# Optimization experiments

Hardware: AMD Instinct MI355X
Metric: run time of the kernel (lower is better)

## Reference

```python
import jax, jax.numpy as jnp
import numpy as np

# ---- larq ste_sign: forward = sign (0 -> +1), backward = clipped straight-through ----
def _sign(x):
    return jnp.where(x >= 0, jnp.ones_like(x), -jnp.ones_like(x))

@jax.custom_vjp
def ste_sign(x):
    return _sign(x)

def _ste_fwd(x):
    return _sign(x), x

def _ste_bwd(x, g):
    return (g * (jnp.abs(x) <= 1.0).astype(g.dtype),)

ste_sign.defvjp(_ste_fwd, _ste_bwd)

BN_EPS = 1e-3  # keras BatchNormalization default epsilon

def conv2d(x, w, padding):
    # x: NHWC, w: HWIO
    return jax.lax.conv_general_dilated(
        x, w, window_strides=(1, 1), padding=padding,
        dimension_numbers=('NHWC', 'HWIO', 'NHWC'))

def maxpool2(x):
    return jax.lax.reduce_window(x, -jnp.inf, jax.lax.max,
                                 (1, 2, 2, 1), (1, 2, 2, 1), 'VALID')

def batchnorm(x, mean, var, beta):
    # BatchNormalization(scale=False): gamma fixed at 1
    return (x - mean) * jax.lax.rsqrt(var + BN_EPS) + beta


def setup_inputs() -> dict:
    key = jax.random.key(0)
    ks = jax.random.split(key, 20)
    d = {}
    d['x'] = jax.random.normal(ks[0], (64, 128, 128, 3), dtype=jnp.float32)
    d['w1'] = jax.random.normal(ks[1], (3, 3, 3, 32), dtype=jnp.float32)
    d['m1'] = jax.random.normal(ks[2], (32,), dtype=jnp.float32)
    d['v1'] = jax.random.uniform(ks[3], (32,), dtype=jnp.float32)
    d['b1'] = jax.random.normal(ks[4], (32,), dtype=jnp.float32)
    d['w2'] = jax.random.normal(ks[5], (3, 3, 32, 64), dtype=jnp.float32)
    d['m2'] = jax.random.normal(ks[6], (64,), dtype=jnp.float32)
    d['v2'] = jax.random.uniform(ks[7], (64,), dtype=jnp.float32)
    d['b2'] = jax.random.normal(ks[8], (64,), dtype=jnp.float32)
    d['w3'] = jax.random.normal(ks[9], (3, 3, 64, 128), dtype=jnp.float32)
    d['m3'] = jax.random.normal(ks[10], (128,), dtype=jnp.float32)
    d['v3'] = jax.random.uniform(ks[11], (128,), dtype=jnp.float32)
    d['b3'] = jax.random.normal(ks[12], (128,), dtype=jnp.float32)
    d['w4'] = jax.random.normal(ks[13], (3, 3, 128, 256), dtype=jnp.float32)
    d['m4'] = jax.random.normal(ks[14], (256,), dtype=jnp.float32)
    d['v4'] = jax.random.uniform(ks[15], (256,), dtype=jnp.float32)
    d['b4'] = jax.random.normal(ks[16], (256,), dtype=jnp.float32)
    return d


def reference(x, w1, m1, v1, b1, w2, m2, v2, b2, w3, m3, v3, b3, w4, m4, v4, b4):
    # Stem: QuantConv2D(32,3x3,valid) with kernel quantized only (no input quantizer)
    y = conv2d(x, ste_sign(w1), 'VALID')          # [B,126,126,32]
    y = batchnorm(maxpool2(y), m1, v1, b1)        # [B,63,63,32]
    # Three binarized blocks: ste_sign(input) conv ste_sign(kernel), same padding
    for w, m, v, b in ((w2, m2, v2, b2), (w3, m3, v3, b3), (w4, m4, v4, b4)):
        y = conv2d(ste_sign(y), ste_sign(w), 'SAME')
        y = batchnorm(maxpool2(y), m, v, b)       # halves spatial dims
    return y                                      # [B,7,7,256]
```

## Files before the change

### kernel.cpp

```cpp
#include <hip/hip_runtime.h>
#include <stdint.h>

#define BN_EPS 1e-3f

template <int CIN, int COUT>
__device__ inline void packw(const float* __restrict__ w, uint32_t* __restrict__ wp, int idx) {
    const int CINW = CIN / 32;
    int co = idx % COUT;
    int t2 = idx / COUT;
    int wi = t2 % CINW;
    int tap = t2 / CINW;
    uint32_t word = 0;
#pragma unroll
    for (int bb = 0; bb < 32; bb++) {
        float val = w[((tap * CIN) + wi * 32 + bb) * COUT + co];
        word |= (uint32_t)(val < 0.f) << bb;
    }
    wp[idx] = word;
}

__global__ void pack_all(const float* __restrict__ w1, const float* __restrict__ w2,
                         const float* __restrict__ w3, const float* __restrict__ w4,
                         float* __restrict__ w1sg, uint32_t* __restrict__ w2p,
                         uint32_t* __restrict__ w3p, uint32_t* __restrict__ w4p) {
    int idx = blockIdx.x * 256 + threadIdx.x;
    if (idx < 864) { w1sg[idx] = (w1[idx] >= 0.f) ? 1.f : -1.f; return; }
    idx -= 864;
    if (idx < 576) { packw<32, 64>(w2, w2p, idx); return; }
    idx -= 576;
    if (idx < 2304) { packw<64, 128>(w3, w3p, idx); return; }
    idx -= 2304;
    if (idx < 9216) { packw<128, 256>(w4, w4p, idx); return; }
}

__global__ __launch_bounds__(256) void conv1_k(const float* __restrict__ x,
                                               const float* __restrict__ wsg,
                                               const float* __restrict__ m1,
                                               const float* __restrict__ v1,
                                               const float* __restrict__ b1,
                                               uint32_t* __restrict__ y1p) {
    __shared__ float xt[18 * 102];
    __shared__ uint32_t half0[128];

    int tile = blockIdx.x;
    int tx = tile & 3; int t2 = tile >> 2;
    int ty = t2 & 7;  int n = t2 >> 3;
    int ph0 = ty * 8, pw0 = tx * 16;
    int r0 = 2 * ph0;
    int cf0 = (2 * pw0) * 3;

    for (int i = threadIdx.x; i < 18 * 102; i += 256) {
        int r = i / 102, c = i % 102;
        int gr = r0 + r, gcf = cf0 + c;
        float vv = 0.f;
        if (gr < 128 && gcf < 384)
            vv = x[(size_t)(n * 128 + gr) * 384 + gcf];
        xt[i] = vv;
    }
    __syncthreads();

    int wave = threadIdx.x >> 6, lane = threadIdx.x & 63;
    int grp = wave & 1;
    int chunk = wave >> 1;
    int px = lane & 15, py = (chunk << 2) + (lane >> 4);
    int ph = ph0 + py, pw = pw0 + px;

    float win[48];
#pragma unroll
    for (int r = 0; r < 4; r++)
#pragma unroll
        for (int cc = 0; cc < 12; cc++)
            win[r * 12 + cc] = xt[(2 * py + r) * 102 + px * 6 + cc];

    const float* wg = wsg + grp * 16;
    uint32_t word = 0;
    for (int csub = 0; csub < 4; csub++) {
        float a[4][4];
#pragma unroll
        for (int j = 0; j < 4; j++)
#pragma unroll
            for (int p = 0; p < 4; p++) a[j][p] = 0.f;
#pragma unroll
        for (int kh = 0; kh < 3; kh++)
#pragma unroll
            for (int kw = 0; kw < 3; kw++)
#pragma unroll
                for (int ci = 0; ci < 3; ci++) {
                    int tap = (kh * 3 + kw) * 3 + ci;
                    float x00 = win[kh * 12 + kw * 3 + ci];
                    float x01 = win[kh * 12 + (kw + 1) * 3 + ci];
                    float x10 = win[(kh + 1) * 12 + kw * 3 + ci];
                    float x11 = win[(kh + 1) * 12 + (kw + 1) * 3 + ci];
#pragma unroll
                    for (int j = 0; j < 4; j++) {
                        float w = wg[tap * 32 + csub * 4 + j];
                        a[j][0] += x00 * w;
                        a[j][1] += x01 * w;
                        a[j][2] += x10 * w;
                        a[j][3] += x11 * w;
                    }
                }
#pragma unroll
        for (int j = 0; j < 4; j++) {
            float mx = fmaxf(fmaxf(a[j][0], a[j][1]), fmaxf(a[j][2], a[j][3]));
            int ch = grp * 16 + csub * 4 + j;
            float y = (mx - m1[ch]) * rsqrtf(v1[ch] + BN_EPS) + b1[ch];
            word |= (uint32_t)(y < 0.f) << (csub * 4 + j);
        }
    }

    int pix = chunk * 64 + lane;
    if (grp == 0) half0[pix] = word;
    __syncthreads();
    if (grp == 1 && ph < 63 && pw < 63)
        y1p[(n * 63 + ph) * 63 + pw] = half0[pix] | (word << 16);
}

__global__ __launch_bounds__(256) void bconv2(const uint32_t* __restrict__ y1p,
                                              const uint32_t* __restrict__ w2p,
                                              const float* __restrict__ m,
                                              const float* __restrict__ v,
                                              const float* __restrict__ b,
                                              uint2* __restrict__ y2p) {
    int wid = __builtin_amdgcn_readfirstlane(blockIdx.x * 4 + (threadIdx.x >> 6));
    int lane = threadIdx.x & 63;
    int pw = wid % 31;
    int t = wid / 31;
    int ph = t % 31;
    int n = t / 31;

    uint32_t wq[9];
#pragma unroll
    for (int tap = 0; tap < 9; tap++) wq[tap] = w2p[tap * 64 + lane];

    int best;
    if (ph > 0 && pw > 0) {
        const uint32_t* p = y1p + (n * 63 + (2 * ph - 1)) * 63 + (2 * pw - 1);
        uint32_t win[16];
#pragma unroll
        for (int r = 0; r < 4; r++)
#pragma unroll
            for (int c = 0; c < 4; c++)
                win[r * 4 + c] = p[r * 63 + c];
        int a0 = 0, a1 = 0, a2 = 0, a3 = 0;
#pragma unroll
        for (int kh = 0; kh < 3; kh++)
#pragma unroll
            for (int kw = 0; kw < 3; kw++) {
                uint32_t w = wq[kh * 3 + kw];
                a0 += __popc(win[kh * 4 + kw] ^ w);
                a1 += __popc(win[kh * 4 + kw + 1] ^ w);
                a2 += __popc(win[(kh + 1) * 4 + kw] ^ w);
                a3 += __popc(win[(kh + 1) * 4 + kw + 1] ^ w);
            }
        best = max(max(288 - 2 * a0, 288 - 2 * a1), max(288 - 2 * a2, 288 - 2 * a3));
    } else {
        best = -1000000;
#pragma unroll
        for (int dy = 0; dy < 2; dy++)
#pragma unroll
            for (int dx = 0; dx < 2; dx++) {
                int oh = 2 * ph + dy, ow = 2 * pw + dx;
                int acc = 0, K = 0;
                for (int kh = 0; kh < 3; kh++) {
                    int ih = oh - 1 + kh;
                    if (ih < 0 || ih >= 63) continue;
                    for (int kw = 0; kw < 3; kw++) {
                        int iw = ow - 1 + kw;
                        if (iw < 0 || iw >= 63) continue;
                        acc += __popc(y1p[(n * 63 + ih) * 63 + iw] ^ wq[kh * 3 + kw]);
                        K += 32;
                    }
                }
                best = max(best, K - 2 * acc);
            }
    }
    float y = ((float)best - m[lane]) * rsqrtf(v[lane] + BN_EPS) + b[lane];
    unsigned long long bal = __ballot(y < 0.f);
    if (lane == 0) y2p[wid] = make_uint2((uint32_t)bal, (uint32_t)(bal >> 32));
}

__global__ __launch_bounds__(256) void bconv3(const uint2* __restrict__ y2p,
                                              const uint32_t* __restrict__ w3p,
                                              const float* __restrict__ m,
                                              const float* __restrict__ v,
                                              const float* __restrict__ b,
                                              uint32_t* __restrict__ y3p) {
    int gwid = __builtin_amdgcn_readfirstlane(blockIdx.x * 4 + (threadIdx.x >> 6));
    int lane = threadIdx.x & 63;
    int half = gwid & 1;
    int pixel = gwid >> 1;
    int co = half * 64 + lane;
    int pw = pixel % 15;
    int t = pixel / 15;
    int ph = t % 15;
    int n = t / 15;

    uint32_t wq0[9], wq1[9];
#pragma unroll
    for (int tap = 0; tap < 9; tap++) {
        wq0[tap] = w3p[(tap * 2 + 0) * 128 + co];
        wq1[tap] = w3p[(tap * 2 + 1) * 128 + co];
    }

    int best;
    if (ph > 0 && pw > 0) {
        const uint2* p = y2p + (n * 31 + (2 * ph - 1)) * 31 + (2 * pw - 1);
        uint2 win[16];
#pragma unroll
        for (int r = 0; r < 4; r++)
#pragma unroll
            for (int c = 0; c < 4; c++)
                win[r * 4 + c] = p[r * 31 + c];
        int a0 = 0, a1 = 0, a2 = 0, a3 = 0;
#pragma unroll
        for (int kh = 0; kh < 3; kh++)
#pragma unroll
            for (int kw = 0; kw < 3; kw++) {
                int tap = kh * 3 + kw;
                uint32_t u0 = wq0[tap], u1 = wq1[tap];
                a0 += __popc(win[kh * 4 + kw].x ^ u0) + __popc(win[kh * 4 + kw].y ^ u1);
                a1 += __popc(win[kh * 4 + kw + 1].x ^ u0) + __popc(win[kh * 4 + kw + 1].y ^ u1);
                a2 += __popc(win[(kh + 1) * 4 + kw].x ^ u0) + __popc(win[(kh + 1) * 4 + kw].y ^ u1);
                a3 += __popc(win[(kh + 1) * 4 + kw + 1].x ^ u0) + __popc(win[(kh + 1) * 4 + kw + 1].y ^ u1);
            }
        best = max(max(576 - 2 * a0, 576 - 2 * a1), max(576 - 2 * a2, 576 - 2 * a3));
    } else {
        best = -1000000;
#pragma unroll
        for (int dy = 0; dy < 2; dy++)
#pragma unroll
            for (int dx = 0; dx < 2; dx++) {
                int oh = 2 * ph + dy, ow = 2 * pw + dx;
                int acc = 0, K = 0;
                for (int kh = 0; kh < 3; kh++) {
                    int ih = oh - 1 + kh;
                    if (ih < 0 || ih >= 31) continue;
                    for (int kw = 0; kw < 3; kw++) {
                        int iw = ow - 1 + kw;
                        if (iw < 0 || iw >= 31) continue;
                        uint2 iv = y2p[(n * 31 + ih) * 31 + iw];
                        int tap = kh * 3 + kw;
                        acc += __popc(iv.x ^ wq0[tap]) + __popc(iv.y ^ wq1[tap]);
                        K += 64;
                    }
                }
                best = max(best, K - 2 * acc);
            }
    }
    float y = ((float)best - m[co]) * rsqrtf(v[co] + BN_EPS) + b[co];
    unsigned long long bal = __ballot(y < 0.f);
    if (lane == 0) {
        y3p[pixel * 4 + half * 2 + 0] = (uint32_t)bal;
        y3p[pixel * 4 + half * 2 + 1] = (uint32_t)(bal >> 32);
    }
}

__global__ __launch_bounds__(256) void bconv4(const uint4* __restrict__ y3p,
                                              const uint32_t* __restrict__ w4p,
                                              const float* __restrict__ m,
                                              const float* __restrict__ v,
                                              const float* __restrict__ b,
                                              float* __restrict__ out) {
    int pixel = blockIdx.x;
    int lane = threadIdx.x & 63;
    int co = (threadIdx.x >> 6) * 64 + lane;
    int pw = pixel % 7;
    int t = pixel / 7;
    int ph = t % 7;
    int n = t / 7;

    uint4 wq[9];
#pragma unroll
    for (int tap = 0; tap < 9; tap++) {
        wq[tap].x = w4p[(tap * 4 + 0) * 256 + co];
        wq[tap].y = w4p[(tap * 4 + 1) * 256 + co];
        wq[tap].z = w4p[(tap * 4 + 2) * 256 + co];
        wq[tap].w = w4p[(tap * 4 + 3) * 256 + co];
    }

    int best;
    if (ph > 0 && pw > 0) {
        const uint4* p = y3p + (n * 15 + (2 * ph - 1)) * 15 + (2 * pw - 1);
        int a0 = 0, a1 = 0, a2 = 0, a3 = 0;
#pragma unroll
        for (int r = 0; r < 4; r++)
#pragma unroll
            for (int c = 0; c < 4; c++) {
                uint4 iv = p[r * 15 + c];
#pragma unroll
                for (int kh = 0; kh < 3; kh++) {
                    int dy = r - kh;
                    if (dy < 0 || dy > 1) continue;
#pragma unroll
                    for (int kw = 0; kw < 3; kw++) {
                        int dx = c - kw;
                        if (dx < 0 || dx > 1) continue;
                        int tap = kh * 3 + kw;
                        int pc = __popc(iv.x ^ wq[tap].x) + __popc(iv.y ^ wq[tap].y)
                               + __popc(iv.z ^ wq[tap].z) + __popc(iv.w ^ wq[tap].w);
                        if (dy == 0 && dx == 0) a0 += pc;
                        else if (dy == 0) a1 += pc;
                        else if (dx == 0) a2 += pc;
                        else a3 += pc;
                    }
                }
            }
        best = max(max(1152 - 2 * a0, 1152 - 2 * a1), max(1152 - 2 * a2, 1152 - 2 * a3));
    } else {
        best = -1000000;
#pragma unroll
        for (int dy = 0; dy < 2; dy++)
#pragma unroll
            for (int dx = 0; dx < 2; dx++) {
                int oh = 2 * ph + dy, ow = 2 * pw + dx;
                int acc = 0, K = 0;
                for (int kh = 0; kh < 3; kh++) {
                    int ih = oh - 1 + kh;
                    if (ih < 0 || ih >= 15) continue;
                    for (int kw = 0; kw < 3; kw++) {
                        int iw = ow - 1 + kw;
                        if (iw < 0 || iw >= 15) continue;
                        uint4 iv = y3p[(n * 15 + ih) * 15 + iw];
                        int tap = kh * 3 + kw;
                        acc += __popc(iv.x ^ wq[tap].x) + __popc(iv.y ^ wq[tap].y)
                             + __popc(iv.z ^ wq[tap].z) + __popc(iv.w ^ wq[tap].w);
                        K += 128;
                    }
                }
                best = max(best, K - 2 * acc);
            }
    }
    float y = ((float)best - m[co]) * rsqrtf(v[co] + BN_EPS) + b[co];
    out[pixel * 256 + co] = y;
}

extern "C" void kernel_launch(void* const* d_in, const int* in_sizes, int n_in,
                              void* d_out, int out_size, void* d_ws, size_t ws_size,
                              hipStream_t stream) {
    const float* x  = (const float*)d_in[0];
    const float* w1 = (const float*)d_in[1];
    const float* m1 = (const float*)d_in[2];
    const float* v1 = (const float*)d_in[3];
    const float* b1 = (const float*)d_in[4];
    const float* w2 = (const float*)d_in[5];
    const float* m2 = (const float*)d_in[6];
    const float* v2 = (const float*)d_in[7];
    const float* b2 = (const float*)d_in[8];
    const float* w3 = (const float*)d_in[9];
    const float* m3 = (const float*)d_in[10];
    const float* v3 = (const float*)d_in[11];
    const float* b3 = (const float*)d_in[12];
    const float* w4 = (const float*)d_in[13];
    const float* m4 = (const float*)d_in[14];
    const float* v4 = (const float*)d_in[15];
    const float* b4 = (const float*)d_in[16];
    float* out = (float*)d_out;

    char* ws = (char*)d_ws;
    size_t off = 0;
    auto take = [&](size_t bytes) -> char* {
        char* p = ws + off;
        off += (bytes + 255) & ~(size_t)255;
        return p;
    };
    uint32_t* y1p  = (uint32_t*)take((size_t)64 * 63 * 63 * 4);
    uint2*    y2p  = (uint2*)take((size_t)64 * 31 * 31 * 8);
    uint32_t* y3p  = (uint32_t*)take((size_t)64 * 15 * 15 * 16);
    float*    w1sg = (float*)take(864 * 4);
    uint32_t* w2p  = (uint32_t*)take(576 * 4);
    uint32_t* w3p  = (uint32_t*)take(2304 * 4);
    uint32_t* w4p  = (uint32_t*)take(9216 * 4);

    pack_all<<<(12960 + 255) / 256, 256, 0, stream>>>(w1, w2, w3, w4, w1sg, w2p, w3p, w4p);

    conv1_k<<<64 * 32, 256, 0, stream>>>(x, w1sg, m1, v1, b1, y1p);

    bconv2<<<(64 * 31 * 31) / 4, 256, 0, stream>>>(y1p, w2p, m2, v2, b2, y2p);

    bconv3<<<(64 * 15 * 15 * 2) / 4, 256, 0, stream>>>(y2p, w3p, m3, v3, b3, y3p);

    bconv4<<<64 * 7 * 7, 256, 0, stream>>>((const uint4*)y3p, w4p, m4, v4, b4, out);
}
```

Before: 182.2 us.

## Pack conv1 weights as sign bitmasks and process multiple pixels per wave

The stem conv now reads its weight signs from 27 wavefront-uniform bitmask words held in scalar registers instead of from a float array. Each thread computes all 32 channels over a tile twice as tall, which removes the shared-memory half-word merge and its extra barrier. bconv2 and bconv3 now have each wave compute 4 (or 2) adjacent pooled outputs from one shared input window, reusing the overlapping columns across them and cutting per-wave setup and weight loads. The cost is more registers per thread, fewer blocks, and clamped-column window loads at the tile edges.

```diff
diff --git a/kernel.cpp b/kernel.cpp
--- a/kernel.cpp
+++ b/kernel.cpp
@@ -21,11 +21,18 @@
 
 __global__ void pack_all(const float* __restrict__ w1, const float* __restrict__ w2,
                          const float* __restrict__ w3, const float* __restrict__ w4,
-                         float* __restrict__ w1sg, uint32_t* __restrict__ w2p,
+                         uint32_t* __restrict__ w1m, uint32_t* __restrict__ w2p,
                          uint32_t* __restrict__ w3p, uint32_t* __restrict__ w4p) {
     int idx = blockIdx.x * 256 + threadIdx.x;
-    if (idx < 864) { w1sg[idx] = (w1[idx] >= 0.f) ? 1.f : -1.f; return; }
-    idx -= 864;
+    if (idx < 27) {
+        uint32_t word = 0;
+#pragma unroll
+        for (int c = 0; c < 32; c++)
+            word |= (uint32_t)(w1[idx * 32 + c] < 0.f) << c;
+        w1m[idx] = word;
+        return;
+    }
+    idx -= 27;
     if (idx < 576) { packw<32, 64>(w2, w2p, idx); return; }
     idx -= 576;
     if (idx < 2304) { packw<64, 128>(w3, w3p, idx); return; }
@@ -34,47 +41,55 @@
 }
 
 __global__ __launch_bounds__(256) void conv1_k(const float* __restrict__ x,
-                                               const float* __restrict__ wsg,
+                                               const uint32_t* __restrict__ w1m,
                                                const float* __restrict__ m1,
                                                const float* __restrict__ v1,
                                                const float* __restrict__ b1,
                                                uint32_t* __restrict__ y1p) {
-    __shared__ float xt[18 * 102];
-    __shared__ uint32_t half0[128];
+    __shared__ float xt[34 * 104];
 
     int tile = blockIdx.x;
-    int tx = tile & 3; int t2 = tile >> 2;
-    int ty = t2 & 7;  int n = t2 >> 3;
-    int ph0 = ty * 8, pw0 = tx * 16;
+    int tx = tile & 3;
+    int ty = (tile >> 2) & 3;
+    int n  = tile >> 4;
+    int ph0 = ty * 16, pw0 = tx * 16;
     int r0 = 2 * ph0;
-    int cf0 = (2 * pw0) * 3;
-
-    for (int i = threadIdx.x; i < 18 * 102; i += 256) {
+    int cf0 = pw0 * 6;
+
+    for (int i = threadIdx.x; i < 34 * 102; i += 256) {
         int r = i / 102, c = i % 102;
         int gr = r0 + r, gcf = cf0 + c;
         float vv = 0.f;
         if (gr < 128 && gcf < 384)
             vv = x[(size_t)(n * 128 + gr) * 384 + gcf];
-        xt[i] = vv;
-    }
+        xt[r * 104 + c] = vv;
+    }
+
+    uint32_t um[27];
+#pragma unroll
+    for (int t = 0; t < 27; t++)
+        um[t] = __builtin_amdgcn_readfirstlane(w1m[t]);
+
     __syncthreads();
 
     int wave = threadIdx.x >> 6, lane = threadIdx.x & 63;
-    int grp = wave & 1;
-    int chunk = wave >> 1;
-    int px = lane & 15, py = (chunk << 2) + (lane >> 4);
+    int px = lane & 15, py = (wave << 2) + (lane >> 4);
     int ph = ph0 + py, pw = pw0 + px;
 
     float win[48];
 #pragma unroll
-    for (int r = 0; r < 4; r++)
-#pragma unroll
-        for (int cc = 0; cc < 12; cc++)
-            win[r * 12 + cc] = xt[(2 * py + r) * 102 + px * 6 + cc];
-
-    const float* wg = wsg + grp * 16;
+    for (int r = 0; r < 4; r++) {
+        const float2* bp = (const float2*)&xt[(2 * py + r) * 104 + 6 * px];
+#pragma unroll
+        for (int q = 0; q < 6; q++) {
+            float2 f2 = bp[q];
+            win[r * 12 + 2 * q]     = f2.x;
+            win[r * 12 + 2 * q + 1] = f2.y;
+        }
+    }
+
     uint32_t word = 0;
-    for (int csub = 0; csub < 4; csub++) {
+    for (int cg = 0; cg < 8; cg++) {
         float a[4][4];
 #pragma unroll
         for (int j = 0; j < 4; j++)
@@ -91,9 +106,10 @@
                     float x01 = win[kh * 12 + (kw + 1) * 3 + ci];
                     float x10 = win[(kh + 1) * 12 + kw * 3 + ci];
                     float x11 = win[(kh + 1) * 12 + (kw + 1) * 3 + ci];
+                    uint32_t mw = um[tap];
 #pragma unroll
                     for (int j = 0; j < 4; j++) {
-                        float w = wg[tap * 32 + csub * 4 + j];
+                        float w = (mw & (1u << (cg * 4 + j))) ? -1.f : 1.f;
                         a[j][0] += x00 * w;
                         a[j][1] += x01 * w;
                         a[j][2] += x10 * w;
@@ -103,17 +119,14 @@
 #pragma unroll
         for (int j = 0; j < 4; j++) {
             float mx = fmaxf(fmaxf(a[j][0], a[j][1]), fmaxf(a[j][2], a[j][3]));
-            int ch = grp * 16 + csub * 4 + j;
+            int ch = cg * 4 + j;
             float y = (mx - m1[ch]) * rsqrtf(v1[ch] + BN_EPS) + b1[ch];
-            word |= (uint32_t)(y < 0.f) << (csub * 4 + j);
-        }
-    }
-
-    int pix = chunk * 64 + lane;
-    if (grp == 0) half0[pix] = word;
-    __syncthreads();
-    if (grp == 1 && ph < 63 && pw < 63)
-        y1p[(n * 63 + ph) * 63 + pw] = half0[pix] | (word << 16);
+            word |= (uint32_t)(y < 0.f) << ch;
+        }
+    }
+
+    if (ph < 63 && pw < 63)
+        y1p[(n * 63 + ph) * 63 + pw] = word;
 }
 
 __global__ __launch_bounds__(256) void bconv2(const uint32_t* __restrict__ y1p,
@@ -122,62 +135,90 @@
                                               const float* __restrict__ v,
                                               const float* __restrict__ b,
                                               uint2* __restrict__ y2p) {
-    int wid = __builtin_amdgcn_readfirstlane(blockIdx.x * 4 + (threadIdx.x >> 6));
+    int gw = __builtin_amdgcn_readfirstlane(blockIdx.x * 4 + (threadIdx.x >> 6));
     int lane = threadIdx.x & 63;
-    int pw = wid % 31;
-    int t = wid / 31;
+    int pwg = gw & 7;
+    int t = gw >> 3;
     int ph = t % 31;
     int n = t / 31;
 
     uint32_t wq[9];
 #pragma unroll
     for (int tap = 0; tap < 9; tap++) wq[tap] = w2p[tap * 64 + lane];
-
-    int best;
-    if (ph > 0 && pw > 0) {
-        const uint32_t* p = y1p + (n * 63 + (2 * ph - 1)) * 63 + (2 * pw - 1);
-        uint32_t win[16];
+    float mm = m[lane], vv = v[lane], bb = b[lane];
+
+    uint2 o0, o1, o2, o3;
+
+    if (ph > 0 && pwg > 0) {
+        int row0 = 2 * ph - 1, col0 = 8 * pwg - 1;
+        uint32_t win[4][10];
 #pragma unroll
         for (int r = 0; r < 4; r++)
 #pragma unroll
-            for (int c = 0; c < 4; c++)
-                win[r * 4 + c] = p[r * 63 + c];
-        int a0 = 0, a1 = 0, a2 = 0, a3 = 0;
-#pragma unroll
-        for (int kh = 0; kh < 3; kh++)
-#pragma unroll
-            for (int kw = 0; kw < 3; kw++) {
-                uint32_t w = wq[kh * 3 + kw];
-                a0 += __popc(win[kh * 4 + kw] ^ w);
-                a1 += __popc(win[kh * 4 + kw + 1] ^ w);
-                a2 += __popc(win[(kh + 1) * 4 + kw] ^ w);
-                a3 += __popc(win[(kh + 1) * 4 + kw + 1] ^ w);
+            for (int c = 0; c < 10; c++)
+                win[r][c] = y1p[(n * 63 + row0 + r) * 63 + min(col0 + c, 62)];
+
+        uint2 res[4];
+#pragma unroll
+        for (int p = 0; p < 4; p++) {
+            int a0 = 0, a1 = 0, a2 = 0, a3 = 0;
+#pragma unroll
+            for (int kh = 0; kh < 3; kh++)
+#pragma unroll
+                for (int kw = 0; kw < 3; kw++) {
+                    uint32_t w = wq[kh * 3 + kw];
+                    a0 += __popc(win[kh][2 * p + kw] ^ w);
+                    a1 += __popc(win[kh][2 * p + kw + 1] ^ w);
+                    a2 += __popc(win[kh + 1][2 * p + kw] ^ w);
+                    a3 += __popc(win[kh + 1][2 * p + kw + 1] ^ w);
+                }
+            int mn = min(min(a0, a1), min(a2, a3));
+            int best = 288 - 2 * mn;
+            float y = ((float)best - mm) * rsqrtf(vv + BN_EPS) + bb;
+            unsigned long long bal = __ballot(y < 0.f);
+            res[p] = make_uint2((uint32_t)bal, (uint32_t)(bal >> 32));
+        }
+        o0 = res[0]; o1 = res[1]; o2 = res[2]; o3 = res[3];
+    } else {
+        uint2 res[4];
+#pragma unroll
+        for (int p = 0; p < 4; p++) {
+            int pw = 4 * pwg + p;
+            int best = -1000000;
+            if (pw < 31) {
+#pragma unroll
+                for (int dy = 0; dy < 2; dy++)
+#pragma unroll
+                    for (int dx = 0; dx < 2; dx++) {
+                        int oh = 2 * ph + dy, ow = 2 * pw + dx;
+                        int acc = 0, K = 0;
+                        for (int kh = 0; kh < 3; kh++) {
+                            int ih = oh - 1 + kh;
+                            if (ih < 0 || ih >= 63) continue;
+                            for (int kw = 0; kw < 3; kw++) {
+                                int iw = ow - 1 + kw;
+                                if (iw < 0 || iw >= 63) continue;
+                                acc += __popc(y1p[(n * 63 + ih) * 63 + iw] ^ wq[kh * 3 + kw]);
+                                K += 32;
+                            }
+                        }
+                        best = max(best, K - 2 * acc);
+                    }
             }
-        best = max(max(288 - 2 * a0, 288 - 2 * a1), max(288 - 2 * a2, 288 - 2 * a3));
-    } else {
-        best = -1000000;
-#pragma unroll
-        for (int dy = 0; dy < 2; dy++)
-#pragma unroll
-            for (int dx = 0; dx < 2; dx++) {
-                int oh = 2 * ph + dy, ow = 2 * pw + dx;
-                int acc = 0, K = 0;
-                for (int kh = 0; kh < 3; kh++) {
-                    int ih = oh - 1 + kh;
-                    if (ih < 0 || ih >= 63) continue;
-                    for (int kw = 0; kw < 3; kw++) {
-                        int iw = ow - 1 + kw;
-                        if (iw < 0 || iw >= 63) continue;
-                        acc += __popc(y1p[(n * 63 + ih) * 63 + iw] ^ wq[kh * 3 + kw]);
-                        K += 32;
-                    }
-                }
-                best = max(best, K - 2 * acc);
-            }
-    }
-    float y = ((float)best - m[lane]) * rsqrtf(v[lane] + BN_EPS) + b[lane];
-    unsigned long long bal = __ballot(y < 0.f);
-    if (lane == 0) y2p[wid] = make_uint2((uint32_t)bal, (uint32_t)(bal >> 32));
+            float y = ((float)best - mm) * rsqrtf(vv + BN_EPS) + bb;
+            unsigned long long bal = __ballot(y < 0.f);
+            res[p] = make_uint2((uint32_t)bal, (uint32_t)(bal >> 32));
+        }
+        o0 = res[0]; o1 = res[1]; o2 = res[2]; o3 = res[3];
+    }
+
+    uint2 rr = o0;
+    if (lane == 1) rr = o1;
+    if (lane == 2) rr = o2;
+    if (lane == 3) rr = o3;
+    int pws = 4 * pwg + lane;
+    if (lane < 4 && pws < 31)
+        y2p[(n * 31 + ph) * 31 + pws] = rr;
 }
 
 __global__ __launch_bounds__(256) void bconv3(const uint2* __restrict__ y2p,
@@ -186,15 +227,15 @@
                                               const float* __restrict__ v,
                                               const float* __restrict__ b,
                                               uint32_t* __restrict__ y3p) {
-    int gwid = __builtin_amdgcn_readfirstlane(blockIdx.x * 4 + (threadIdx.x >> 6));
+    int gw = __builtin_amdgcn_readfirstlane(blockIdx.x * 4 + (threadIdx.x >> 6));
     int lane = threadIdx.x & 63;
-    int half = gwid & 1;
-    int pixel = gwid >> 1;
-    int co = half * 64 + lane;
-    int pw = pixel % 15;
-    int t = pixel / 15;
+    int half = gw & 1;
+    int t = gw >> 1;
+    int pwg = t & 7;
+    t >>= 3;
     int ph = t % 15;
     int n = t / 15;
+    int co = half * 64 + lane;
 
     uint32_t wq0[9], wq1[9];
 #pragma unroll
@@ -202,57 +243,83 @@
         wq0[tap] = w3p[(tap * 2 + 0) * 128 + co];
         wq1[tap] = w3p[(tap * 2 + 1) * 128 + co];
     }
-
-    int best;
-    if (ph > 0 && pw > 0) {
-        const uint2* p = y2p + (n * 31 + (2 * ph - 1)) * 31 + (2 * pw - 1);
-        uint2 win[16];
+    float mm = m[co], vv = v[co], bb = b[co];
+
+    unsigned long long bal0, bal1;
+
+    if (ph > 0 && pwg > 0) {
+        int row0 = 2 * ph - 1, col0 = 4 * pwg - 1;
+        uint2 win[4][6];
 #pragma unroll
         for (int r = 0; r < 4; r++)
 #pragma unroll
-            for (int c = 0; c < 4; c++)
-                win[r * 4 + c] = p[r * 31 + c];
-        int a0 = 0, a1 = 0, a2 = 0, a3 = 0;
-#pragma unroll
-        for (int kh = 0; kh < 3; kh++)
-#pragma unroll
-            for (int kw = 0; kw < 3; kw++) {
-                int tap = kh * 3 + kw;
-                uint32_t u0 = wq0[tap], u1 = wq1[tap];
-                a0 += __popc(win[kh * 4 + kw].x ^ u0) + __popc(win[kh * 4 + kw].y ^ u1);
-                a1 += __popc(win[kh * 4 + kw + 1].x ^ u0) + __popc(win[kh * 4 + kw + 1].y ^ u1);
-                a2 += __popc(win[(kh + 1) * 4 + kw].x ^ u0) + __popc(win[(kh + 1) * 4 + kw].y ^ u1);
-                a3 += __popc(win[(kh + 1) * 4 + kw + 1].x ^ u0) + __popc(win[(kh + 1) * 4 + kw + 1].y ^ u1);
+            for (int c = 0; c < 6; c++)
+                win[r][c] = y2p[(n * 31 + row0 + r) * 31 + min(col0 + c, 30)];
+
+        unsigned long long bals[2];
+#pragma unroll
+        for (int p = 0; p < 2; p++) {
+            int a0 = 0, a1 = 0, a2 = 0, a3 = 0;
+#pragma unroll
+            for (int kh = 0; kh < 3; kh++)
+#pragma unroll
+                for (int kw = 0; kw < 3; kw++) {
+                    int tap = kh * 3 + kw;
+                    uint32_t u0 = wq0[tap], u1 = wq1[tap];
+                    a0 += __popc(win[kh][2 * p + kw].x ^ u0) + __popc(win[kh][2 * p + kw].y ^ u1);
+                    a1 += __popc(win[kh][2 * p + kw + 1].x ^ u0) + __popc(win[kh][2 * p + kw + 1].y ^ u1);
+                    a2 += __popc(win[kh + 1][2 * p + kw].x ^ u0) + __popc(win[kh + 1][2 * p + kw].y ^ u1);
+                    a3 += __popc(win[kh + 1][2 * p + kw + 1].x ^ u0) + __popc(win[kh + 1][2 * p + kw + 1].y ^ u1);
+                }
+            int mn = min(min(a0, a1), min(a2, a3));
+            int best = 576 - 2 * mn;
+            float y = ((float)best - mm) * rsqrtf(vv + BN_EPS) + bb;
+            bals[p] = __ballot(y < 0.f);
+        }
+        bal0 = bals[0]; bal1 = bals[1];
+    } else {
+        unsigned long long bals[2];
+#pragma unroll
+        for (int p = 0; p < 2; p++) {
+            int pw = 2 * pwg + p;
+            int best = -1000000;
+            if (pw < 15) {
+#pragma unroll
+                for (int dy = 0; dy < 2; dy++)
+#pragma unroll
+                    for (int dx = 0; dx < 2; dx++) {
+                        int oh = 2 * ph + dy, ow = 2 * pw + dx;
+                        int acc = 0, K = 0;
+                        for (int kh = 0; kh < 3; kh++) {
+                            int ih = oh - 1 + kh;
+                            if (ih < 0 || ih >= 31) continue;
+                            for (int kw = 0; kw < 3; kw++) {
+                                int iw = ow - 1 + kw;
+                                if (iw < 0 || iw >= 31) continue;
+                                uint2 iv = y2p[(n * 31 + ih) * 31 + iw];
+                                int tap = kh * 3 + kw;
+                                acc += __popc(iv.x ^ wq0[tap]) + __popc(iv.y ^ wq1[tap]);
+                                K += 64;
+                            }
+                        }
+                        best = max(best, K - 2 * acc);
+                    }
             }
-        best = max(max(576 - 2 * a0, 576 - 2 * a1), max(576 - 2 * a2, 576 - 2 * a3));
-    } else {
-        best = -1000000;
-#pragma unroll
-        for (int dy = 0; dy < 2; dy++)
-#pragma unroll
-            for (int dx = 0; dx < 2; dx++) {
-                int oh = 2 * ph + dy, ow = 2 * pw + dx;
-                int acc = 0, K = 0;
-                for (int kh = 0; kh < 3; kh++) {
-                    int ih = oh - 1 + kh;
-                    if (ih < 0 || ih >= 31) continue;
-                    for (int kw = 0; kw < 3; kw++) {
-                        int iw = ow - 1 + kw;
-                        if (iw < 0 || iw >= 31) continue;
-                        uint2 iv = y2p[(n * 31 + ih) * 31 + iw];
-                        int tap = kh * 3 + kw;
-                        acc += __popc(iv.x ^ wq0[tap]) + __popc(iv.y ^ wq1[tap]);
-                        K += 64;
-                    }
-                }
-                best = max(best, K - 2 * acc);
-            }
-    }
-    float y = ((float)best - m[co]) * rsqrtf(v[co] + BN_EPS) + b[co];
-    unsigned long long bal = __ballot(y < 0.f);
-    if (lane == 0) {
-        y3p[pixel * 4 + half * 2 + 0] = (uint32_t)bal;
-        y3p[pixel * 4 + half * 2 + 1] = (uint32_t)(bal >> 32);
+            float y = ((float)best - mm) * rsqrtf(vv + BN_EPS) + bb;
+            bals[p] = __ballot(y < 0.f);
+        }
+        bal0 = bals[0]; bal1 = bals[1];
+    }
+
+    uint32_t val = (uint32_t)bal0;
+    if (lane == 1) val = (uint32_t)(bal0 >> 32);
+    if (lane == 2) val = (uint32_t)bal1;
+    if (lane == 3) val = (uint32_t)(bal1 >> 32);
+    int p = lane >> 1;
+    int pw = 2 * pwg + p;
+    if (lane < 4 && pw < 15) {
+        int pixel = (n * 15 + ph) * 15 + pw;
+        y3p[pixel * 4 + half * 2 + (lane & 1)] = val;
     }
 }
 
@@ -364,21 +431,21 @@
         off += (bytes + 255) & ~(size_t)255;
         return p;
     };
-    uint32_t* y1p  = (uint32_t*)take((size_t)64 * 63 * 63 * 4);
-    uint2*    y2p  = (uint2*)take((size_t)64 * 31 * 31 * 8);
-    uint32_t* y3p  = (uint32_t*)take((size_t)64 * 15 * 15 * 16);
-    float*    w1sg = (float*)take(864 * 4);
-    uint32_t* w2p  = (uint32_t*)take(576 * 4);
-    uint32_t* w3p  = (uint32_t*)take(2304 * 4);
-    uint32_t* w4p  = (uint32_t*)take(9216 * 4);
-
-    pack_all<<<(12960 + 255) / 256, 256, 0, stream>>>(w1, w2, w3, w4, w1sg, w2p, w3p, w4p);
-
-    conv1_k<<<64 * 32, 256, 0, stream>>>(x, w1sg, m1, v1, b1, y1p);
-
-    bconv2<<<(64 * 31 * 31) / 4, 256, 0, stream>>>(y1p, w2p, m2, v2, b2, y2p);
-
-    bconv3<<<(64 * 15 * 15 * 2) / 4, 256, 0, stream>>>(y2p, w3p, m3, v3, b3, y3p);
+    uint32_t* y1p = (uint32_t*)take((size_t)64 * 63 * 63 * 4);
+    uint2*    y2p = (uint2*)take((size_t)64 * 31 * 31 * 8);
+    uint32_t* y3p = (uint32_t*)take((size_t)64 * 15 * 15 * 16);
+    uint32_t* w1m = (uint32_t*)take(27 * 4);
+    uint32_t* w2p = (uint32_t*)take(576 * 4);
+    uint32_t* w3p = (uint32_t*)take(2304 * 4);
+    uint32_t* w4p = (uint32_t*)take(9216 * 4);
+
+    pack_all<<<(12123 + 255) / 256, 256, 0, stream>>>(w1, w2, w3, w4, w1m, w2p, w3p, w4p);
+
+    conv1_k<<<64 * 16, 256, 0, stream>>>(x, w1m, m1, v1, b1, y1p);
+
+    bconv2<<<(64 * 31 * 8) / 4, 256, 0, stream>>>(y1p, w2p, m2, v2, b2, y2p);
+
+    bconv3<<<(64 * 15 * 8 * 2) / 4, 256, 0, stream>>>(y2p, w3p, m3, v3, b3, y3p);
 
     bconv4<<<64 * 7 * 7, 256, 0, stream>>>((const uint4*)y3p, w4p, m4, v4, b4, out);
 }
```

New measurement: 170.8 us. -6.3%, faster.
